# Optimization experiments

Hardware: AMD Instinct MI355X
Metric: run time of the kernel (lower is better)

Reference implementation:

```python
import jax, jax.numpy as jnp
import numpy as np

C, G, S, L, B = 16, 8192, 8, 3, 32


def setup_inputs() -> dict:
    key = jax.random.key(0)
    kx, kI = jax.random.split(key)
    # x: valuation vector over G ground atoms per batch element, in [0,1)
    x = jax.random.uniform(kx, (B, G), dtype=jnp.float32)
    # I: precomputed index tensor [C, G, S, L], indices into the G axis of x
    I = jax.random.randint(kI, (C, G, S, L), 0, G, dtype=jnp.int64)
    return {"x": x, "I": I}


def reference(x, I):
    # Equivalent of: for each clause i, gather(V_tild, 1, I_i) -> prod over L -> sum over S
    # torch gather semantics: out[b, g, s, l] = x[b, I[i, g, s, l]]
    # Vectorized over all clauses at once; no repeat/broadcast materialization beyond the gather.
    gathered = x[:, I]                        # [B, C, G, S, L]
    body = jnp.prod(gathered, axis=-1)        # conjunction over L body literals -> [B, C, G, S]
    clause_val = jnp.sum(body, axis=-1)       # sum over S substitutions -> [B, C, G]
    # torch.stack over clauses puts C first: [C, B, G]
    return jnp.transpose(clause_val, (1, 0, 2))
```

## Files before the change

### kernel.cpp

```cpp
#include <hip/hip_runtime.h>
#include <hip/hip_fp16.h>
#include <stdint.h>

#define Cc 16
#define Gg 8192
#define Ss 8
#define Ll 3
#define Bb 32

#define BH 4
#define NZ (Bb / BH)
#define MTHREADS 512

#define XH_BYTES  ((size_t)NZ * Gg * BH * 2)
#define I16_OFF   XH_BYTES
#define I16_BYTES ((size_t)Cc * Gg * Ss * Ll * 2)

#define PB_X 64
#define PB_I 384
__global__ __launch_bounds__(256) void prepass(const float* __restrict__ x,
                                               const uint4* __restrict__ I4,
                                               uint4* __restrict__ ws4) {
    const int bid = blockIdx.x;
    if (bid < PB_X) {
        const int tt = bid * 256 + threadIdx.x;
        const int zh = tt >> 11;
        const int gg = (tt & 2047) << 2;
        const float* xr = x + (size_t)(4 * zh) * Gg + gg;
        float4 f0 = *(const float4*)&xr[0];
        float4 f1 = *(const float4*)&xr[Gg];
        float4 f2 = *(const float4*)&xr[2 * (size_t)Gg];
        float4 f3 = *(const float4*)&xr[3 * (size_t)Gg];
        __half2 lo0 = __floats2half2_rn(f0.x, f1.x), hi0 = __floats2half2_rn(f2.x, f3.x);
        __half2 lo1 = __floats2half2_rn(f0.y, f1.y), hi1 = __floats2half2_rn(f2.y, f3.y);
        __half2 lo2 = __floats2half2_rn(f0.z, f1.z), hi2 = __floats2half2_rn(f2.z, f3.z);
        __half2 lo3 = __floats2half2_rn(f0.w, f1.w), hi3 = __floats2half2_rn(f2.w, f3.w);
        uint4 w0 = make_uint4(*(uint32_t*)&lo0, *(uint32_t*)&hi0,
                              *(uint32_t*)&lo1, *(uint32_t*)&hi1);
        uint4 w1 = make_uint4(*(uint32_t*)&lo2, *(uint32_t*)&hi2,
                              *(uint32_t*)&lo3, *(uint32_t*)&hi3);
        uint4* dst = ws4 + ((size_t)zh << 12) + ((size_t)(tt & 2047) << 1);
        dst[0] = w0;
        dst[1] = w1;
    } else {
        const int t = (bid - PB_X) * 256 + threadIdx.x;
        uint2* ow = (uint2*)((char*)ws4 + I16_OFF);
        #pragma unroll
        for (int i = 0; i < 8; ++i) {
            const int e = t + i * (PB_I * 256);
            uint4 v = I4[e];
            uint2 o;
            o.x = (v.x & 0xffffu) | (v.y << 16);
            o.y = (v.z & 0xffffu) | (v.w << 16);
            ow[e] = o;
        }
    }
}

__device__ __forceinline__ void clause_eval16(const uint2* __restrict__ xl2,
                                              const uint4 q[3], float acc[4]) {
    const uint32_t u[12] = {q[0].x, q[0].y, q[0].z, q[0].w,
                            q[1].x, q[1].y, q[1].z, q[1].w,
                            q[2].x, q[2].y, q[2].z, q[2].w};
    #pragma unroll
    for (int h = 0; h < 2; ++h) {
        uint2 r[12];
        #pragma unroll
        for (int m = 0; m < 6; ++m) {
            const uint32_t w = u[6 * h + m];
            r[2 * m]     = xl2[w & 0xffffu];
            r[2 * m + 1] = xl2[w >> 16];
        }
        #pragma unroll
        for (int s = 0; s < 4; ++s) {
            const uint2 ra = r[3 * s + 0];
            const uint2 rb = r[3 * s + 1];
            const uint2 rd = r[3 * s + 2];
            __half2 p0 = __hmul2(__hmul2(*(const __half2*)&ra.x,
                                         *(const __half2*)&rb.x),
                                 *(const __half2*)&rd.x);
            __half2 p1 = __hmul2(__hmul2(*(const __half2*)&ra.y,
                                         *(const __half2*)&rb.y),
                                 *(const __half2*)&rd.y);
            float2 f0 = __half22float2(p0);
            float2 f1 = __half22float2(p1);
            acc[0] += f0.x;
            acc[1] += f0.y;
            acc[2] += f1.x;
            acc[3] += f1.y;
        }
    }
}

#define QLOAD(QB, CV, GV)                                                     \
    {                                                                         \
        const uint4* p =                                                      \
            (const uint4*)(i16 + ((size_t)(CV) * Gg + (GV)) * (Ss * Ll));     \
        QB[0] = p[0]; QB[1] = p[1]; QB[2] = p[2];                             \
    }

#define EVAL_STORE(QB, CV, GV)                                                \
    {                                                                         \
        float acc[4] = {0.f, 0.f, 0.f, 0.f};                                  \
        clause_eval16(xl2, QB, acc);                                          \
        float* op = out + ((size_t)((CV) * Bb + BH * zh)) * Gg + (GV);        \
        __builtin_nontemporal_store(acc[0], &op[0]);                          \
        __builtin_nontemporal_store(acc[1], &op[(size_t)Gg]);                 \
        __builtin_nontemporal_store(acc[2], &op[2 * (size_t)Gg]);             \
        __builtin_nontemporal_store(acc[3], &op[3 * (size_t)Gg]);             \
    }

__global__ __launch_bounds__(MTHREADS, 4) void clause_m(
        const uint4* __restrict__ xh4, const ushort* __restrict__ i16,
        float* __restrict__ out) {
    __shared__ uint4 xl4[Gg / 2];
    const int tid = threadIdx.x;

    const int lb = (blockIdx.x & 7) * 64 + (blockIdx.x >> 3);
    const int zh = lb & (NZ - 1);
    const int combo = lb >> 3;
    const int gc = combo & 7;
    const int cp = combo >> 3;
    const int gbase = gc * 1024;
    const int c0 = 2 * cp, c1 = 2 * cp + 1;
    const int g0 = gbase + tid;
    const int g1 = gbase + MTHREADS + tid;

    const uint4* src = xh4 + ((size_t)zh << 12);
    uint4 st[8];
    #pragma unroll
    for (int i = 0; i < 8; ++i) st[i] = src[tid + i * MTHREADS];

    uint4 qA[3], qB[3], qC[3], qD[3];
    QLOAD(qA, c0, g0)
    QLOAD(qB, c0, g1)
    QLOAD(qC, c1, g0)
    QLOAD(qD, c1, g1)

    #pragma unroll
    for (int i = 0; i < 8; ++i) xl4[tid + i * MTHREADS] = st[i];

    __syncthreads();

    const uint2* xl2 = (const uint2*)xl4;
    EVAL_STORE(qA, c0, g0)
    EVAL_STORE(qB, c0, g1)
    EVAL_STORE(qC, c1, g0)
    EVAL_STORE(qD, c1, g1)
}

__global__ __launch_bounds__(256) void clause_kernel_direct(const float* __restrict__ x,
                                                            const int* __restrict__ I,
                                                            float* __restrict__ out) {
    const int tid = threadIdx.x;
    const int b = tid & 31;
    const int j = tid >> 5;
    const int g = blockIdx.x * 8 + j;
    const int c = blockIdx.y;

    const int* Icg = I + (size_t)(c * Gg + g) * (Ss * Ll);
    float sum = 0.f;
    #pragma unroll
    for (int s = 0; s < Ss; ++s) {
        float p0 = x[(size_t)b * Gg + Icg[3 * s + 0]];
        float p1 = x[(size_t)b * Gg + Icg[3 * s + 1]];
        float p2 = x[(size_t)b * Gg + Icg[3 * s + 2]];
        sum += p0 * p1 * p2;
    }
    out[(size_t)(c * Bb + b) * Gg + g] = sum;
}

extern "C" void kernel_launch(void* const* d_in, const int* in_sizes, int n_in,
                              void* d_out, int out_size, void* d_ws, size_t ws_size,
                              hipStream_t stream) {
    const float* x = (const float*)d_in[0];
    const int* I = (const int*)d_in[1];
    float* out = (float*)d_out;

    const size_t need = I16_OFF + I16_BYTES;
    if (ws_size >= need) {
        prepass<<<PB_X + PB_I, 256, 0, stream>>>(x, (const uint4*)I,
                                                 (uint4*)d_ws);
        clause_m<<<512, MTHREADS, 0, stream>>>(
            (const uint4*)d_ws, (const ushort*)((char*)d_ws + I16_OFF), out);
    } else {
        clause_kernel_direct<<<dim3(Gg / 8, Cc), 256, 0, stream>>>(x, I, out);
    }
}
```

Before: 78.91 us.

## Fuse prepass and clause evaluation into one cooperative kernel with grid sync

Merges the separate conversion prepass (x to packed fp16, int64 indices to uint16) and the clause evaluation kernel into a single cooperative launch separated by a grid-wide barrier. The goal is to remove the second kernel launch and the gap between the two kernels. In exchange it adds grid sync overhead, requires all 512 blocks to be co-resident, and keeps the two-kernel path as a fallback if the cooperative launch fails.

```diff
diff --git a/kernel.cpp b/kernel.cpp
--- a/kernel.cpp
+++ b/kernel.cpp
@@ -1,6 +1,9 @@
 #include <hip/hip_runtime.h>
 #include <hip/hip_fp16.h>
+#include <hip/hip_cooperative_groups.h>
 #include <stdint.h>
+
+namespace cg = cooperative_groups;
 
 #define Cc 16
 #define Gg 8192
@@ -11,50 +14,32 @@
 #define BH 4
 #define NZ (Bb / BH)
 #define MTHREADS 512
+#define NBLK 512
 
 #define XH_BYTES  ((size_t)NZ * Gg * BH * 2)
 #define I16_OFF   XH_BYTES
 #define I16_BYTES ((size_t)Cc * Gg * Ss * Ll * 2)
 
-#define PB_X 64
-#define PB_I 384
-__global__ __launch_bounds__(256) void prepass(const float* __restrict__ x,
-                                               const uint4* __restrict__ I4,
-                                               uint4* __restrict__ ws4) {
-    const int bid = blockIdx.x;
-    if (bid < PB_X) {
-        const int tt = bid * 256 + threadIdx.x;
-        const int zh = tt >> 11;
-        const int gg = (tt & 2047) << 2;
-        const float* xr = x + (size_t)(4 * zh) * Gg + gg;
-        float4 f0 = *(const float4*)&xr[0];
-        float4 f1 = *(const float4*)&xr[Gg];
-        float4 f2 = *(const float4*)&xr[2 * (size_t)Gg];
-        float4 f3 = *(const float4*)&xr[3 * (size_t)Gg];
-        __half2 lo0 = __floats2half2_rn(f0.x, f1.x), hi0 = __floats2half2_rn(f2.x, f3.x);
-        __half2 lo1 = __floats2half2_rn(f0.y, f1.y), hi1 = __floats2half2_rn(f2.y, f3.y);
-        __half2 lo2 = __floats2half2_rn(f0.z, f1.z), hi2 = __floats2half2_rn(f2.z, f3.z);
-        __half2 lo3 = __floats2half2_rn(f0.w, f1.w), hi3 = __floats2half2_rn(f2.w, f3.w);
-        uint4 w0 = make_uint4(*(uint32_t*)&lo0, *(uint32_t*)&hi0,
-                              *(uint32_t*)&lo1, *(uint32_t*)&hi1);
-        uint4 w1 = make_uint4(*(uint32_t*)&lo2, *(uint32_t*)&hi2,
-                              *(uint32_t*)&lo3, *(uint32_t*)&hi3);
-        uint4* dst = ws4 + ((size_t)zh << 12) + ((size_t)(tt & 2047) << 1);
-        dst[0] = w0;
-        dst[1] = w1;
-    } else {
-        const int t = (bid - PB_X) * 256 + threadIdx.x;
-        uint2* ow = (uint2*)((char*)ws4 + I16_OFF);
-        #pragma unroll
-        for (int i = 0; i < 8; ++i) {
-            const int e = t + i * (PB_I * 256);
-            uint4 v = I4[e];
-            uint2 o;
-            o.x = (v.x & 0xffffu) | (v.y << 16);
-            o.y = (v.z & 0xffffu) | (v.w << 16);
-            ow[e] = o;
-        }
-    }
+__device__ __forceinline__ void build_ximage(const float* __restrict__ x,
+                                             uint4* __restrict__ ws4, int tt) {
+    const int zh = tt >> 11;
+    const int gg = (tt & 2047) << 2;
+    const float* xr = x + (size_t)(4 * zh) * Gg + gg;
+    float4 f0 = *(const float4*)&xr[0];
+    float4 f1 = *(const float4*)&xr[Gg];
+    float4 f2 = *(const float4*)&xr[2 * (size_t)Gg];
+    float4 f3 = *(const float4*)&xr[3 * (size_t)Gg];
+    __half2 lo0 = __floats2half2_rn(f0.x, f1.x), hi0 = __floats2half2_rn(f2.x, f3.x);
+    __half2 lo1 = __floats2half2_rn(f0.y, f1.y), hi1 = __floats2half2_rn(f2.y, f3.y);
+    __half2 lo2 = __floats2half2_rn(f0.z, f1.z), hi2 = __floats2half2_rn(f2.z, f3.z);
+    __half2 lo3 = __floats2half2_rn(f0.w, f1.w), hi3 = __floats2half2_rn(f2.w, f3.w);
+    uint4 w0 = make_uint4(*(uint32_t*)&lo0, *(uint32_t*)&hi0,
+                          *(uint32_t*)&lo1, *(uint32_t*)&hi1);
+    uint4 w1 = make_uint4(*(uint32_t*)&lo2, *(uint32_t*)&hi2,
+                          *(uint32_t*)&lo3, *(uint32_t*)&hi3);
+    uint4* dst = ws4 + ((size_t)zh << 12) + ((size_t)(tt & 2047) << 1);
+    dst[0] = w0;
+    dst[1] = w1;
 }
 
 __device__ __forceinline__ void clause_eval16(const uint2* __restrict__ xl2,
@@ -110,12 +95,11 @@
         __builtin_nontemporal_store(acc[3], &op[3 * (size_t)Gg]);             \
     }
 
-__global__ __launch_bounds__(MTHREADS, 4) void clause_m(
-        const uint4* __restrict__ xh4, const ushort* __restrict__ i16,
-        float* __restrict__ out) {
-    __shared__ uint4 xl4[Gg / 2];
+__device__ __forceinline__ void phase2_eval(const uint4* __restrict__ xh4,
+                                            const ushort* __restrict__ i16,
+                                            float* __restrict__ out,
+                                            uint4* __restrict__ xl4) {
     const int tid = threadIdx.x;
-
     const int lb = (blockIdx.x & 7) * 64 + (blockIdx.x >> 3);
     const int zh = lb & (NZ - 1);
     const int combo = lb >> 3;
@@ -149,6 +133,62 @@
     EVAL_STORE(qD, c1, g1)
 }
 
+__global__ __launch_bounds__(MTHREADS, 4) void fused(
+        const float* __restrict__ x, const uint4* __restrict__ I4,
+        uint4* __restrict__ ws4, float* __restrict__ out) {
+    __shared__ uint4 xl4[Gg / 2];
+    const int t = blockIdx.x * MTHREADS + threadIdx.x;
+
+    {
+        uint2* ow = (uint2*)((char*)ws4 + I16_OFF);
+        #pragma unroll
+        for (int i = 0; i < 3; ++i) {
+            const int e = t + i * (NBLK * MTHREADS);
+            uint4 v = I4[e];
+            uint2 o;
+            o.x = (v.x & 0xffffu) | (v.y << 16);
+            o.y = (v.z & 0xffffu) | (v.w << 16);
+            ow[e] = o;
+        }
+    }
+    if (t < 16384) build_ximage(x, ws4, t);
+
+    __threadfence();
+    cg::this_grid().sync();
+
+    phase2_eval(ws4, (const ushort*)((char*)ws4 + I16_OFF), out, xl4);
+}
+
+#define PB_X 64
+#define PB_I 384
+__global__ __launch_bounds__(256) void prepass(const float* __restrict__ x,
+                                               const uint4* __restrict__ I4,
+                                               uint4* __restrict__ ws4) {
+    const int bid = blockIdx.x;
+    if (bid < PB_X) {
+        build_ximage(x, ws4, bid * 256 + threadIdx.x);
+    } else {
+        const int t = (bid - PB_X) * 256 + threadIdx.x;
+        uint2* ow = (uint2*)((char*)ws4 + I16_OFF);
+        #pragma unroll
+        for (int i = 0; i < 8; ++i) {
+            const int e = t + i * (PB_I * 256);
+            uint4 v = I4[e];
+            uint2 o;
+            o.x = (v.x & 0xffffu) | (v.y << 16);
+            o.y = (v.z & 0xffffu) | (v.w << 16);
+            ow[e] = o;
+        }
+    }
+}
+
+__global__ __launch_bounds__(MTHREADS, 4) void clause_m(
+        const uint4* __restrict__ xh4, const ushort* __restrict__ i16,
+        float* __restrict__ out) {
+    __shared__ uint4 xl4[Gg / 2];
+    phase2_eval(xh4, i16, out, xl4);
+}
+
 __global__ __launch_bounds__(256) void clause_kernel_direct(const float* __restrict__ x,
                                                             const int* __restrict__ I,
                                                             float* __restrict__ out) {
@@ -179,10 +219,19 @@
 
     const size_t need = I16_OFF + I16_BYTES;
     if (ws_size >= need) {
-        prepass<<<PB_X + PB_I, 256, 0, stream>>>(x, (const uint4*)I,
-                                                 (uint4*)d_ws);
-        clause_m<<<512, MTHREADS, 0, stream>>>(
-            (const uint4*)d_ws, (const ushort*)((char*)d_ws + I16_OFF), out);
+        const float* xa = x;
+        const uint4* I4 = (const uint4*)I;
+        uint4* ws4 = (uint4*)d_ws;
+        float* oa = out;
+        void* args[] = {(void*)&xa, (void*)&I4, (void*)&ws4, (void*)&oa};
+        hipError_t err = hipLaunchCooperativeKernel(
+            (const void*)fused, dim3(NBLK), dim3(MTHREADS), args, 0, stream);
+        if (err != hipSuccess) {
+            prepass<<<PB_X + PB_I, 256, 0, stream>>>(x, (const uint4*)I,
+                                                     (uint4*)d_ws);
+            clause_m<<<NBLK, MTHREADS, 0, stream>>>(
+                (const uint4*)d_ws, (const ushort*)((char*)d_ws + I16_OFF), out);
+        }
     } else {
         clause_kernel_direct<<<dim3(Gg / 8, Cc), 256, 0, stream>>>(x, I, out);
     }
```

Result: slower. 214.0 us (+171.2%).
